# Performance work log

Hardware: AMD Instinct MI355X
Metric: run time of the kernel (lower is better)

## Reference

```python
import jax, jax.numpy as jnp
import numpy as np

T, B, E, H = 2048, 2, 1024, 16
D = E // H

def setup_inputs() -> dict:
    key = jax.random.key(0)
    ks = jax.random.split(key, 5)
    s = 1.0 / np.sqrt(E)  # keep projection weights at sane scale
    return {
        "query": jax.random.normal(ks[0], (T, B, E), jnp.float32),
        "Wq": jax.random.normal(ks[1], (E, E), jnp.float32) * s,
        "bq": jnp.zeros((E,), jnp.float32),
        "Wk": jax.random.normal(ks[2], (E, E), jnp.float32) * s,
        "bk": jnp.zeros((E,), jnp.float32),
        "Wv": jax.random.normal(ks[3], (E, E), jnp.float32) * s,
        "bv": jnp.zeros((E,), jnp.float32),
        "Wo": jax.random.normal(ks[4], (E, E), jnp.float32) * s,
        "bo": jnp.zeros((E,), jnp.float32),
    }

def reference(query, Wq, bq, Wk, bk, Wv, bv, Wo, bo):
    # query: [T, B, E] (fairseq time-first). self-attention path.
    scaling = D ** -0.5
    q = (query @ Wq.T + bq) * scaling          # [T,B,E]
    k = query @ Wk.T + bk                      # [T,B,E]
    v = query @ Wv.T + bv                      # [T,B,E]
    # split heads: [T,B,H,D]
    q = q.reshape(T, B, H, D)
    k = k.reshape(T, B, H, D)
    v = v.reshape(T, B, H, D)
    # attention scores [B,H,T,S]
    scores = jnp.einsum("tbhd,sbhd->bhts", q, k)
    probs = jax.nn.softmax(scores, axis=-1)
    # weighted values -> [T,B,H,D]
    attn = jnp.einsum("bhts,sbhd->tbhd", probs, v).reshape(T, B, E)
    return attn @ Wo.T + bo                    # [T,B,E]
```

## Files before the change

### kernel.cpp

```cpp
#include <hip/hip_runtime.h>
#include <hip/hip_bf16.h>

#define T_DIM 2048

typedef __attribute__((ext_vector_type(8))) short short8_t;
typedef short8_t __attribute__((may_alias)) short8_a;
typedef __attribute__((ext_vector_type(4))) short short4_t;
typedef short4_t __attribute__((may_alias)) short4_a;
typedef __attribute__((ext_vector_type(4))) float f32x4;
typedef __attribute__((ext_vector_type(16))) float f32x16;
typedef __attribute__((ext_vector_type(4))) float float4_t;
typedef float4_t __attribute__((may_alias)) float4_a;
typedef __attribute__((ext_vector_type(4))) unsigned int u32x4;

__device__ __forceinline__ short f2bf(float f) {
    unsigned int u = __builtin_bit_cast(unsigned int, f);
    unsigned int r = (u + 0x7fffu + ((u >> 16) & 1u)) >> 16;
    return (short)r;
}

__device__ __forceinline__ void gl_lds16(const short* g, short* l) {
    __builtin_amdgcn_global_load_lds(
        (const __attribute__((address_space(1))) void*)g,
        (__attribute__((address_space(3))) void*)l, 16, 0, 0);
}

__global__ __launch_bounds__(256) void cvt_all(const float* __restrict__ query,
                                               const float* __restrict__ Wq,
                                               const float* __restrict__ Wk,
                                               const float* __restrict__ Wv,
                                               const float* __restrict__ Wo,
                                               short* __restrict__ out) {
    const int bx = blockIdx.x;
    const int i = bx * 2048 + threadIdx.x * 8;
    const float* s;
    if (bx < 2048) {
        s = query + i;
    } else {
        int j = i - 4194304;
        int wsel = j >> 20;
        const float* wp = wsel == 0 ? Wq : (wsel == 1 ? Wk : (wsel == 2 ? Wv : Wo));
        s = wp + (j & 1048575);
    }
    float4_a a = *(const float4_a*)s;
    float4_a b = *(const float4_a*)(s + 4);
    short8_a r;
    r[0] = f2bf(a[0]); r[1] = f2bf(a[1]); r[2] = f2bf(a[2]); r[3] = f2bf(a[3]);
    r[4] = f2bf(b[0]); r[5] = f2bf(b[1]); r[6] = f2bf(b[2]); r[7] = f2bf(b[3]);
    *(short8_a*)(out + i) = r;
}

template <int BM, int BN, int MODE>
__global__ __launch_bounds__(256) void gemm_lds(const short* __restrict__ A,
                                                const short* __restrict__ W,
                                                const float* __restrict__ b0,
                                                const float* __restrict__ b1,
                                                const float* __restrict__ b2,
                                                short* __restrict__ o0,
                                                short* __restrict__ o1,
                                                short* __restrict__ o2,
                                                float* __restrict__ of) {
    constexpr int FM = BM / 32;
    constexpr int FN = BN / 32;
    __shared__ short As[BM * 32];
    __shared__ short Bs[BN * 32];

    const int tid = threadIdx.x;
    const int l = tid & 63, w = tid >> 6;
    const int wm = w >> 1, wn = w & 1;
    const int m0 = blockIdx.y * BM, n0 = blockIdx.x * BN;
    const int l15 = l & 15, l4 = l >> 4;
    const int lr = l >> 2, lc = (l & 3) * 8;

    f32x4 acc[FM][FN];
#pragma unroll
    for (int i = 0; i < FM; i++)
#pragma unroll
        for (int j = 0; j < FN; j++) {
            f32x4 z = {0.f, 0.f, 0.f, 0.f};
            acc[i][j] = z;
        }

    const short* Ab = A + (m0 + lr) * 1024 + lc;
    const short* Wb = W + (n0 + lr) * 1024 + lc;

    for (int k0 = 0; k0 < 1024; k0 += 32) {
#pragma unroll
        for (int j = 0; j < BM / 64; j++) {
            int base = (j * 4 + w) * 16;
            gl_lds16(Ab + base * 1024 + k0, &As[base * 32]);
        }
#pragma unroll
        for (int j = 0; j < BN / 64; j++) {
            int base = (j * 4 + w) * 16;
            gl_lds16(Wb + base * 1024 + k0, &Bs[base * 32]);
        }
        __syncthreads();

        short8_t af[FM], bf[FN];
#pragma unroll
        for (int m = 0; m < FM; m++)
            af[m] = *(const short8_a*)&As[(wm * (BM / 2) + m * 16 + l15) * 32 + l4 * 8];
#pragma unroll
        for (int n = 0; n < FN; n++)
            bf[n] = *(const short8_a*)&Bs[(wn * (BN / 2) + n * 16 + l15) * 32 + l4 * 8];
#pragma unroll
        for (int m = 0; m < FM; m++)
#pragma unroll
            for (int n = 0; n < FN; n++)
                acc[m][n] = __builtin_amdgcn_mfma_f32_16x16x32_bf16(af[m], bf[n], acc[m][n], 0, 0, 0);
        __syncthreads();
    }

    if (MODE == 3) {
#pragma unroll
        for (int n = 0; n < FN; n++) {
            int col = n0 + wn * (BN / 2) + n * 16 + l15;
            float bv = b0[col];
#pragma unroll
            for (int m = 0; m < FM; m++)
#pragma unroll
                for (int i = 0; i < 4; i++) {
                    int row = m0 + wm * (BM / 2) + m * 16 + l4 * 4 + i;
                    of[row * 1024 + col] = acc[m][n][i] + bv;
                }
        }
    } else {
        const int proj = n0 >> 10;
        const float* bias = proj == 0 ? b0 : (proj == 1 ? b1 : b2);
        short* outp = proj == 0 ? o0 : (proj == 1 ? o1 : o2);
#pragma unroll
        for (int n = 0; n < FN; n++) {
            int cw = (n0 + wn * (BN / 2) + n * 16 + l15) & 1023;
            float bv = bias[cw];
            int h = cw >> 6, d = cw & 63;
#pragma unroll
            for (int m = 0; m < FM; m++)
#pragma unroll
                for (int i = 0; i < 4; i++) {
                    int row = m0 + wm * (BM / 2) + m * 16 + l4 * 4 + i;
                    float v = acc[m][n][i] + bv;
                    if (proj == 0) v *= 0.18033688011112042f;
                    int bb = row & 1, t = row >> 1;
                    if (proj == 2)
                        outp[((bb * 16 + h) * 64 + d) * 2048 + t] = f2bf(v);
                    else
                        outp[((bb * 16 + h) * 2048 + t) * 64 + d] = f2bf(v);
                }
        }
    }
}

__device__ __forceinline__ float max16(const f32x16 v) {
    float a0 = fmaxf(fmaxf(v[0], v[1]), v[2]);
    float a1 = fmaxf(fmaxf(v[3], v[4]), v[5]);
    float a2 = fmaxf(fmaxf(v[6], v[7]), v[8]);
    float a3 = fmaxf(fmaxf(v[9], v[10]), v[11]);
    float a4 = fmaxf(fmaxf(v[12], v[13]), v[14]);
    float b0 = fmaxf(fmaxf(a0, a1), v[15]);
    float b1 = fmaxf(fmaxf(a2, a3), a4);
    return fmaxf(b0, b1);
}

__global__ __launch_bounds__(256) void flash_attn(const short* __restrict__ Q,
                                                  const short* __restrict__ K,
                                                  const short* __restrict__ Vt,
                                                  short* __restrict__ O) {
    __shared__ short Ks[2][64 * 64];
    __shared__ short Vs[2][64 * 64];

    const int tid = threadIdx.x, l = tid & 63, w = tid >> 6;
    const int l31 = l & 31, hi = l >> 5;
    const int e = l31 & 7;

    const int bid = blockIdx.x + (blockIdx.y << 4);
    const int swz = (bid & 7) * 64 + (bid >> 3);
    const int qt = swz & 15, bh = swz >> 4;

    const int b = bh >> 4, hh = bh & 15;
    const int qrow = qt * 128 + w * 32 + l31;

    const short* Qp = Q + bh * (T_DIM * 64);
    const short* Kp = K + bh * (T_DIM * 64);
    const short* Vp = Vt + bh * (64 * T_DIM);

    short8_t qf[4];
#pragma unroll
    for (int c = 0; c < 4; c++)
        qf[c] = *(const short8_a*)&Qp[qrow * 64 + c * 16 + hi * 8];

    f32x16 oacc[2];
    f32x16 lacc;
#pragma unroll
    for (int i = 0; i < 16; i++) { oacc[0][i] = 0.f; oacc[1][i] = 0.f; lacc[i] = 0.f; }
    float mrow = -1e30f;

    short8_t ones;
#pragma unroll
    for (int j = 0; j < 8; j++) ones[j] = (short)0x3F80;

    const int lrow = l >> 3;
    const int lch = (l & 7) ^ (lrow & 7);
    const int j0 = 2 * w, j1 = 2 * w + 1;
    const short* kg0 = Kp + (j0 * 8 + lrow) * 64 + lch * 8;
    const short* kg1 = Kp + (j1 * 8 + lrow) * 64 + lch * 8;
    const short* vg0 = Vp + (j0 * 8 + lrow) * 2048 + lch * 8;
    const short* vg1 = Vp + (j1 * 8 + lrow) * 2048 + lch * 8;

    auto stage = [&](int it, int buf) {
        const int koff = it * 4096;
        const int voff = it * 64;
        gl_lds16(kg0 + koff, &Ks[buf][j0 * 512]);
        gl_lds16(kg1 + koff, &Ks[buf][j1 * 512]);
        gl_lds16(vg0 + voff, &Vs[buf][j0 * 512]);
        gl_lds16(vg1 + voff, &Vs[buf][j1 * 512]);
    };

    stage(0, 0);

    for (int it = 0; it < 32; ++it) {
        const int cur = it & 1;
        __syncthreads();
        if (it + 1 < 32) stage(it + 1, cur ^ 1);

        const short* kc = Ks[cur];
        const short* vc = Vs[cur];

        f32x16 st[2];
#pragma unroll
        for (int r = 0; r < 2; r++) {
#pragma unroll
            for (int i = 0; i < 16; i++) st[r][i] = 0.f;
#pragma unroll
            for (int c = 0; c < 4; c++) {
                short8_t kf = *(const short8_a*)&kc[(r * 32 + l31) * 64 + ((2 * c + hi) ^ e) * 8];
                st[r] = __builtin_amdgcn_mfma_f32_32x32x16_bf16(kf, qf[c], st[r], 0, 0, 0);
            }
        }

        float pmax = fmaxf(max16(st[0]), max16(st[1]));
        pmax = fmaxf(pmax, __shfl_xor(pmax, 32));
        if (__any(pmax > mrow + 8.f)) {
            float mn = fmaxf(mrow, pmax);
            float sc = exp2f(mrow - mn);
            mrow = mn;
            lacc[0] *= sc;
#pragma unroll
            for (int dd = 0; dd < 2; dd++)
#pragma unroll
                for (int i = 0; i < 16; i++) oacc[dd][i] *= sc;
        }
#pragma unroll
        for (int r = 0; r < 2; r++)
#pragma unroll
            for (int i = 0; i < 16; i++) st[r][i] = exp2f(st[r][i] - mrow);

#pragma unroll
        for (int r = 0; r < 2; r++) {
            unsigned pk8[8];
#pragma unroll
            for (int u = 0; u < 8; u++) {
                unsigned t;
                asm("v_cvt_pk_bf16_f32 %0, %1, %2" : "=v"(t) : "v"(st[r][2 * u]), "v"(st[r][2 * u + 1]));
                pk8[u] = t;
            }
#pragma unroll
            for (int cc = 0; cc < 2; cc++) {
                unsigned A0 = pk8[4 * cc + 0], B0 = pk8[4 * cc + 2];
                unsigned A1 = pk8[4 * cc + 1], B1 = pk8[4 * cc + 3];
                asm("v_permlane32_swap_b32 %0, %1" : "+v"(A0), "+v"(B0));
                asm("v_permlane32_swap_b32 %0, %1" : "+v"(A1), "+v"(B1));
                u32x4 pu = {A0, A1, B0, B1};
                short8_t pf = __builtin_bit_cast(short8_t, pu);
                lacc = __builtin_amdgcn_mfma_f32_32x32x16_bf16(ones, pf, lacc, 0, 0, 0);
#pragma unroll
                for (int dd = 0; dd < 2; dd++) {
                    short8_t vf = *(const short8_a*)&vc[(dd * 32 + l31) * 64 +
                                                        ((4 * r + 2 * cc + hi) ^ e) * 8];
                    oacc[dd] = __builtin_amdgcn_mfma_f32_32x32x16_bf16(vf, pf, oacc[dd], 0, 0, 0);
                }
            }
        }
    }

    float rl = 1.0f / lacc[0];
#pragma unroll
    for (int dd = 0; dd < 2; dd++)
#pragma unroll
        for (int g = 0; g < 4; g++) {
            short4_t o4;
#pragma unroll
            for (int i = 0; i < 4; i++) o4[i] = f2bf(oacc[dd][4 * g + i] * rl);
            *(short4_a*)&O[(qrow * 2 + b) * 1024 + hh * 64 + dd * 32 + g * 8 + hi * 4] = o4;
        }
}

extern "C" void kernel_launch(void* const* d_in, const int* in_sizes, int n_in,
                              void* d_out, int out_size, void* d_ws, size_t ws_size,
                              hipStream_t stream) {
    const float* query = (const float*)d_in[0];
    const float* Wq = (const float*)d_in[1];
    const float* bq = (const float*)d_in[2];
    const float* Wk = (const float*)d_in[3];
    const float* bk = (const float*)d_in[4];
    const float* Wv = (const float*)d_in[5];
    const float* bv = (const float*)d_in[6];
    const float* Wo = (const float*)d_in[7];
    const float* bo = (const float*)d_in[8];

    short* Xbf = (short*)d_ws;
    short* Wqb = Xbf + 4194304;
    short* Wkb = Wqb + 1048576;
    short* Wvb = Wkb + 1048576;
    short* Wob = Wvb + 1048576;
    short* Qb = Wob + 1048576;
    short* Kb = Qb + 4194304;
    short* Vtb = Kb + 4194304;
    short* attnb = Xbf;

    cvt_all<<<4096, 256, 0, stream>>>(query, Wq, Wk, Wv, Wo, Xbf);

    gemm_lds<128, 128, 4><<<dim3(24, 32), 256, 0, stream>>>(Xbf, Wqb, bq, bk, bv,
                                                            Qb, Kb, Vtb, nullptr);

    flash_attn<<<dim3(16, 32), 256, 0, stream>>>(Qb, Kb, Vtb, attnb);

    gemm_lds<64, 128, 3><<<dim3(8, 64), 256, 0, stream>>>(attnb, Wob, bo, nullptr, nullptr,
                                                          nullptr, nullptr, nullptr, (float*)d_out);
}
```

Measured before the change: 142.1 us.

## Software-pipeline flash attention: overlap QK of next tile with PV of previous

```diff
diff --git a/kernel.cpp b/kernel.cpp
--- a/kernel.cpp
+++ b/kernel.cpp
@@ -166,8 +166,8 @@
                                                   const short* __restrict__ K,
                                                   const short* __restrict__ Vt,
                                                   short* __restrict__ O) {
-    __shared__ short Ks[2][64 * 64];
-    __shared__ short Vs[2][64 * 64];
+    __shared__ short Ks[4][64 * 64];
+    __shared__ short Vs[4][64 * 64];
 
     const int tid = threadIdx.x, l = tid & 63, w = tid >> 6;
     const int l31 = l & 31, hi = l >> 5;
@@ -207,56 +207,52 @@
     const short* vg0 = Vp + (j0 * 8 + lrow) * 2048 + lch * 8;
     const short* vg1 = Vp + (j1 * 8 + lrow) * 2048 + lch * 8;
 
-    auto stage = [&](int it, int buf) {
-        const int koff = it * 4096;
-        const int voff = it * 64;
+    auto stage = [&](int it) {
+        const int buf = it & 3;
+        const int koff = it * 4096, voff = it * 64;
         gl_lds16(kg0 + koff, &Ks[buf][j0 * 512]);
         gl_lds16(kg1 + koff, &Ks[buf][j1 * 512]);
         gl_lds16(vg0 + voff, &Vs[buf][j0 * 512]);
         gl_lds16(vg1 + voff, &Vs[buf][j1 * 512]);
     };
 
-    stage(0, 0);
-
-    for (int it = 0; it < 32; ++it) {
-        const int cur = it & 1;
-        __syncthreads();
-        if (it + 1 < 32) stage(it + 1, cur ^ 1);
-
-        const short* kc = Ks[cur];
-        const short* vc = Vs[cur];
-
-        f32x16 st[2];
+    auto qk = [&](f32x16* st, int t) {
+        const short* kc = &Ks[t & 3][0];
+        f32x16 z;
+#pragma unroll
+        for (int i = 0; i < 16; i++) z[i] = 0.f;
+        st[0] = z; st[1] = z;
+#pragma unroll
+        for (int c = 0; c < 4; c++) {
+            short8_t kf0 = *(const short8_a*)&kc[(l31) * 64 + ((2 * c + hi) ^ e) * 8];
+            short8_t kf1 = *(const short8_a*)&kc[(32 + l31) * 64 + ((2 * c + hi) ^ e) * 8];
+            st[0] = __builtin_amdgcn_mfma_f32_32x32x16_bf16(kf0, qf[c], st[0], 0, 0, 0);
+            st[1] = __builtin_amdgcn_mfma_f32_32x32x16_bf16(kf1, qf[c], st[1], 0, 0, 0);
+        }
+    };
+
+    auto pv = [&](const short8_t* pf, int t) {
+        const short* vc = &Vs[t & 3][0];
+#pragma unroll
+        for (int r = 0; r < 2; r++)
+#pragma unroll
+            for (int cc = 0; cc < 2; cc++) {
+                short8_t p = pf[r * 2 + cc];
+                lacc = __builtin_amdgcn_mfma_f32_32x32x16_bf16(ones, p, lacc, 0, 0, 0);
+#pragma unroll
+                for (int dd = 0; dd < 2; dd++) {
+                    short8_t vf = *(const short8_a*)&vc[(dd * 32 + l31) * 64 +
+                                                        ((4 * r + 2 * cc + hi) ^ e) * 8];
+                    oacc[dd] = __builtin_amdgcn_mfma_f32_32x32x16_bf16(vf, p, oacc[dd], 0, 0, 0);
+                }
+            }
+    };
+
+    auto expack = [&](f32x16* st, short8_t* pf) {
 #pragma unroll
         for (int r = 0; r < 2; r++) {
 #pragma unroll
-            for (int i = 0; i < 16; i++) st[r][i] = 0.f;
-#pragma unroll
-            for (int c = 0; c < 4; c++) {
-                short8_t kf = *(const short8_a*)&kc[(r * 32 + l31) * 64 + ((2 * c + hi) ^ e) * 8];
-                st[r] = __builtin_amdgcn_mfma_f32_32x32x16_bf16(kf, qf[c], st[r], 0, 0, 0);
-            }
-        }
-
-        float pmax = fmaxf(max16(st[0]), max16(st[1]));
-        pmax = fmaxf(pmax, __shfl_xor(pmax, 32));
-        if (__any(pmax > mrow + 8.f)) {
-            float mn = fmaxf(mrow, pmax);
-            float sc = exp2f(mrow - mn);
-            mrow = mn;
-            lacc[0] *= sc;
-#pragma unroll
-            for (int dd = 0; dd < 2; dd++)
-#pragma unroll
-                for (int i = 0; i < 16; i++) oacc[dd][i] *= sc;
-        }
-#pragma unroll
-        for (int r = 0; r < 2; r++)
-#pragma unroll
             for (int i = 0; i < 16; i++) st[r][i] = exp2f(st[r][i] - mrow);
-
-#pragma unroll
-        for (int r = 0; r < 2; r++) {
             unsigned pk8[8];
 #pragma unroll
             for (int u = 0; u < 8; u++) {
@@ -271,17 +267,44 @@
                 asm("v_permlane32_swap_b32 %0, %1" : "+v"(A0), "+v"(B0));
                 asm("v_permlane32_swap_b32 %0, %1" : "+v"(A1), "+v"(B1));
                 u32x4 pu = {A0, A1, B0, B1};
-                short8_t pf = __builtin_bit_cast(short8_t, pu);
-                lacc = __builtin_amdgcn_mfma_f32_32x32x16_bf16(ones, pf, lacc, 0, 0, 0);
-#pragma unroll
-                for (int dd = 0; dd < 2; dd++) {
-                    short8_t vf = *(const short8_a*)&vc[(dd * 32 + l31) * 64 +
-                                                        ((4 * r + 2 * cc + hi) ^ e) * 8];
-                    oacc[dd] = __builtin_amdgcn_mfma_f32_32x32x16_bf16(vf, pf, oacc[dd], 0, 0, 0);
-                }
+                pf[r * 2 + cc] = __builtin_bit_cast(short8_t, pu);
             }
         }
+    };
+
+    f32x16 stA[2], stB[2];
+    short8_t pfA[4], pfB[4];
+
+    stage(0);
+    __syncthreads();
+    stage(1);
+    qk(stB, 0);
+
+    auto halfiter = [&](f32x16* stCur, f32x16* stNext, short8_t* pfIn, short8_t* pfOut, int i) {
+        __syncthreads();
+        if (i + 2 < 32) stage(i + 2);
+        float pmax = fmaxf(max16(stCur[0]), max16(stCur[1]));
+        pmax = fmaxf(pmax, __shfl_xor(pmax, 32));
+        if (i + 1 < 32) qk(stNext, i + 1);
+        if (i > 0) pv(pfIn, i - 1);
+        if (__any(pmax > mrow + 8.f)) {
+            float mn = fmaxf(mrow, pmax);
+            float sc = exp2f(mrow - mn);
+            mrow = mn;
+            lacc[0] *= sc;
+#pragma unroll
+            for (int dd = 0; dd < 2; dd++)
+#pragma unroll
+                for (int ii = 0; ii < 16; ii++) oacc[dd][ii] *= sc;
+        }
+        expack(stCur, pfOut);
+    };
+
+    for (int i = 0; i < 32; i += 2) {
+        halfiter(stB, stA, pfA, pfB, i);
+        halfiter(stA, stB, pfB, pfA, i + 1);
     }
+    pv(pfA, 31);
 
     float rl = 1.0f / lacc[0];
 #pragma unroll
```

Measured after the change: 136.3 us. 4.1% less time.
